# Performance work log

Hardware: AMD Instinct MI355X
Metric: run time of the kernel (lower is better)

The kernel has to match this reference:

```python
import jax, jax.numpy as jnp
import numpy as np

N = 100000        # nodes
E = 3200000       # edges (avg in-degree ~32)
NG = 64           # graphs in batch
F_IN = 64         # num_node_features
AVG_LOG = float(np.log(33.0))   # avg log-degree baked from deg (avg degree 32)
BN_EPS = 1e-5
STD_EPS = 1e-5

def _glorot(key, fi, fo):
    lim = float(np.sqrt(6.0 / (fi + fo)))
    return jax.random.uniform(key, (fi, fo), jnp.float32, -lim, lim)

def setup_inputs():
    key = jax.random.key(0)
    ks = jax.random.split(key, 16)
    inp = {
        'x': jax.random.normal(ks[0], (N, F_IN), jnp.float32),
        'edge_index': jax.random.randint(ks[1], (2, E), 0, N),
        'batch': jnp.sort(jax.random.randint(ks[2], (N,), 0, NG)),
    }
    dims = [(F_IN, 96), (96, 64), (64, 32), (32, 20)]
    for i, (fi, fo) in enumerate(dims):
        inp[f'w{i}'] = _glorot(ks[3 + i], 13 * fi, fo)  # (4 aggr * 3 scalers + 1 self) * F_in
        inp[f'b{i}'] = jnp.zeros((fo,), jnp.float32)
    for i, c in enumerate([96, 64, 20]):
        inp[f'g{i}'] = jnp.ones((c,), jnp.float32)
        inp[f'be{i}'] = jnp.zeros((c,), jnp.float32)
    inp['w_lin'] = _glorot(ks[10], 20, 11)
    inp['b_lin'] = jnp.zeros((11,), jnp.float32)
    return inp

def _pna_layer(x, src, dst, cnt, degc, W, b):
    m = x[src]                                          # [E, F] gather of neighbor feats
    inv = (1.0 / degc)[:, None]
    mean = jax.ops.segment_sum(m, dst, N) * inv
    mean_sq = jax.ops.segment_sum(m * m, dst, N) * inv
    std = jnp.sqrt(jax.nn.relu(mean_sq - mean * mean) + STD_EPS)
    has = (cnt > 0)[:, None]
    mn = jnp.where(has, jax.ops.segment_min(m, dst, N), 0.0)
    mx = jnp.where(has, jax.ops.segment_max(m, dst, N), 0.0)
    agg = jnp.concatenate([mean, mn, mx, std], axis=-1)  # [N, 4F]
    logd = jnp.log(degc + 1.0)[:, None]
    out = jnp.concatenate([agg, agg * (logd / AVG_LOG), agg * (AVG_LOG / logd)], axis=-1)  # [N, 12F]
    out = jnp.concatenate([x, out], axis=-1)             # [N, 13F] self + scaled aggregations
    return out @ W + b

def _bn(x, g, b):
    mu = x.mean(0)
    var = x.var(0)  # biased var: matches torch BatchNorm training forward
    return (x - mu) * jax.lax.rsqrt(var + BN_EPS) * g + b

def _forward(x, edge_index, batch, w0, b0, w1, b1, w2, b2, w3, b3,
             g0, be0, g1, be1, g2, be2, w_lin, b_lin):
    src, dst = edge_index[0], edge_index[1]
    cnt = jax.ops.segment_sum(jnp.ones((E,), x.dtype), dst, N)  # in-degree
    degc = jnp.maximum(cnt, 1.0)
    h = jax.nn.relu(_bn(_pna_layer(x, src, dst, cnt, degc, w0, b0), g0, be0))
    h = jax.nn.relu(_bn(_pna_layer(h, src, dst, cnt, degc, w1, b1), g1, be1))
    h = jax.nn.relu(_pna_layer(h, src, dst, cnt, degc, w2, b2))
    h = _bn(_pna_layer(h, src, dst, cnt, degc, w3, b3), g2, be2)
    gcnt = jnp.maximum(jax.ops.segment_sum(jnp.ones((N,), h.dtype), batch, NG), 1.0)
    z = jax.ops.segment_sum(h, batch, NG) / gcnt[:, None]       # global mean pool [NG, 20]
    out = jax.nn.softmax(z @ w_lin + b_lin, axis=-1)            # dropout identity (eval)
    return out, z

def reference(x, edge_index, batch, w0, b0, w1, b1, w2, b2, w3, b3,
              g0, be0, g1, be1, g2, be2, w_lin, b_lin):
    return _forward(x, edge_index, batch, w0, b0, w1, b1, w2, b2, w3, b3,
                    g0, be0, g1, be1, g2, be2, w_lin, b_lin)
```

## Files before the change

### kernel.cpp

```cpp
#include <hip/hip_runtime.h>

#define NN 100000
#define NGRAPH 64
#define NPART 8
#define NPB 12500
#define DB 16
#define PW_C 2048
#define AVGLOG 3.4965075614664802f

using f32x2 = __attribute__((ext_vector_type(2))) float;
using f32x4 = __attribute__((ext_vector_type(4))) float;
using f16x2 = __attribute__((ext_vector_type(2))) _Float16;
using f16x8 = __attribute__((ext_vector_type(8))) _Float16;
using f16x4 = __attribute__((ext_vector_type(4))) _Float16;
using i32x4 = __attribute__((ext_vector_type(4))) int;

__global__ __launch_bounds__(256) void k_pcnt(const int* __restrict__ ei,
                                              int* __restrict__ pcnt, int E, int W) {
  const int w = blockIdx.x * 4 + (threadIdx.x >> 6);
  const int lane = threadIdx.x & 63;
  if (w >= W) return;
  int c[NPART];
#pragma unroll
  for (int b = 0; b < NPART; ++b) c[b] = 0;
  const long long base = (long long)w * PW_C;
  for (int r = 0; r < PW_C / 256; ++r) {
    long long e0 = base + r * 256 + lane * 4;
    int bk[4] = {-1, -1, -1, -1};
    if (e0 + 3 < E) {
      i32x4 d = __builtin_nontemporal_load((const i32x4*)(ei + E + e0));
#pragma unroll
      for (int k = 0; k < 4; ++k) bk[k] = d[k] / NPB;
    } else {
#pragma unroll
      for (int k = 0; k < 4; ++k)
        if (e0 + k < E) bk[k] = ei[E + e0 + k] / NPB;
    }
#pragma unroll
    for (int b = 0; b < NPART; ++b) {
      int t = 0;
#pragma unroll
      for (int k = 0; k < 4; ++k) t += __popcll(__ballot(bk[k] == b));
      c[b] += t;
    }
  }
  if (lane == 0) {
#pragma unroll
    for (int b = 0; b < NPART; ++b) pcnt[w * NPART + b] = c[b];
  }
}

__global__ void k_pscan(const int* __restrict__ pcnt, int* __restrict__ pbase,
                        int* __restrict__ bcur, int W) {
  __shared__ int s[256];
  __shared__ int btot[NPART];
  const int t = threadIdx.x;
  const int per = (W + 255) / 256;
  for (int b = 0; b < NPART; ++b) {
    int loc = 0;
    const int w0 = t * per;
    for (int i = 0; i < per; ++i) {
      int w = w0 + i;
      if (w < W) loc += pcnt[w * NPART + b];
    }
    s[t] = loc;
    __syncthreads();
    for (int off = 1; off < 256; off <<= 1) {
      int u = (t >= off) ? s[t - off] : 0;
      __syncthreads();
      s[t] += u;
      __syncthreads();
    }
    int run = s[t] - loc;
    if (t == 255) btot[b] = s[255];
    for (int i = 0; i < per; ++i) {
      int w = w0 + i;
      if (w < W) {
        pbase[w * NPART + b] = run;
        run += pcnt[w * NPART + b];
      }
    }
    __syncthreads();
  }
  if (t < NPART) bcur[t] = btot[t];
}

__global__ __launch_bounds__(256) void k_pbin(const int* __restrict__ ei,
                                              const int* __restrict__ pbase,
                                              unsigned long long* __restrict__ bkt,
                                              int cap, int E, int W) {
  const int w = blockIdx.x * 4 + (threadIdx.x >> 6);
  const int lane = threadIdx.x & 63;
  if (w >= W) return;
  int off[NPART];
#pragma unroll
  for (int b = 0; b < NPART; ++b) off[b] = pbase[w * NPART + b];
  const unsigned long long lmask = (1ull << lane) - 1ull;
  const long long base = (long long)w * PW_C;
  for (int r = 0; r < PW_C / 256; ++r) {
    long long e0 = base + r * 256 + lane * 4;
    int bk[4] = {-1, -1, -1, -1};
    int sv[4], dv[4];
    if (e0 + 3 < E) {
      i32x4 d = __builtin_nontemporal_load((const i32x4*)(ei + E + e0));
      i32x4 s4 = __builtin_nontemporal_load((const i32x4*)(ei + e0));
#pragma unroll
      for (int k = 0; k < 4; ++k) { dv[k] = d[k]; sv[k] = s4[k]; bk[k] = d[k] / NPB; }
    } else {
#pragma unroll
      for (int k = 0; k < 4; ++k)
        if (e0 + k < E) { dv[k] = ei[E + e0 + k]; sv[k] = ei[e0 + k]; bk[k] = dv[k] / NPB; }
    }
#pragma unroll
    for (int k = 0; k < 4; ++k) {
#pragma unroll
      for (int b = 0; b < NPART; ++b) {
        unsigned long long m = __ballot(bk[k] == b);
        if (bk[k] == b) {
          int idx = off[b] + __popcll(m & lmask);
          bkt[(size_t)b * cap + idx] =
              ((unsigned long long)(unsigned)dv[k] << 32) | (unsigned)sv[k];
        }
        off[b] += __popcll(m);
      }
    }
  }
}

__global__ __launch_bounds__(256) void k_dhist(
    const unsigned long long* __restrict__ bkt, const int* __restrict__ bcur,
    int cap, int* __restrict__ dhist) {
  __shared__ int hist[NPB];
  const int p = blockIdx.x & (NPART - 1);
  const int b = blockIdx.x >> 3;
  const int tid = threadIdx.x;
  for (int i = tid; i < NPB; i += 256) hist[i] = 0;
  __syncthreads();
  const int n = bcur[p];
  const int chunk = (n + DB - 1) / DB;
  const int lo = b * chunk, hi = min(n, lo + chunk);
  const unsigned long long* base = bkt + (size_t)p * cap;
  const int plo = p * NPB;
  for (int i = lo + tid; i < hi; i += 256) {
    unsigned long long v = base[i];
    atomicAdd(&hist[(int)(v >> 32) - plo], 1);
  }
  __syncthreads();
  int* dst = dhist + ((size_t)p * DB + b) * NPB;
  for (int i = tid; i < NPB; i += 256) dst[i] = hist[i];
}

__global__ void k_mergesum(int* __restrict__ dhist, int* __restrict__ cnt,
                           int* __restrict__ bsum, int n) {
  __shared__ int s[256];
  int i = blockIdx.x * 256 + threadIdx.x;
  int acc = 0;
  if (i < n) {
    int p = i / NPB, li = i - p * NPB;
    int* hb = dhist + (size_t)p * DB * NPB + li;
#pragma unroll
    for (int b = 0; b < DB; ++b) {
      int t = hb[b * NPB];
      hb[b * NPB] = acc;
      acc += t;
    }
    cnt[i] = acc;
  }
  s[threadIdx.x] = acc;
  __syncthreads();
  for (int off = 128; off > 0; off >>= 1) {
    if (threadIdx.x < off) s[threadIdx.x] += s[threadIdx.x + off];
    __syncthreads();
  }
  if (threadIdx.x == 0) bsum[blockIdx.x] = s[0];
}

__global__ __launch_bounds__(256) void k_binfill(
    const unsigned long long* __restrict__ bkt, const int* __restrict__ bcur,
    int cap, const int* __restrict__ dhist, const int* __restrict__ row_ptr,
    int* __restrict__ colv) {
  __shared__ int rank[NPB];
  const int p = blockIdx.x & (NPART - 1);
  const int b = blockIdx.x >> 3;
  const int tid = threadIdx.x;
  const int plo = p * NPB;
  const int* soff = dhist + ((size_t)p * DB + b) * NPB;
  for (int li = tid; li < NPB; li += 256) rank[li] = row_ptr[plo + li] + soff[li];
  __syncthreads();
  const int n = bcur[p];
  const int chunk = (n + DB - 1) / DB;
  const int lo = b * chunk, hi = min(n, lo + chunk);
  const unsigned long long* base = bkt + (size_t)p * cap;
  for (int i = lo + tid; i < hi; i += 256) {
    unsigned long long v = base[i];
    int d = (int)(v >> 32);
    int s = (int)(v & 0xffffffffu);
    int pos = atomicAdd(&rank[d - plo], 1);
    colv[pos] = s;
  }
}

__global__ void k_scanb(const int* __restrict__ bsum, int* __restrict__ boff, int nb) {
  __shared__ int s[512];
  int t = threadIdx.x;
  int v = (t < nb) ? bsum[t] : 0;
  s[t] = v;
  __syncthreads();
  for (int off = 1; off < 512; off <<= 1) {
    int u = (t >= off) ? s[t - off] : 0;
    __syncthreads();
    s[t] += u;
    __syncthreads();
  }
  if (t < nb) boff[t] = s[t] - v;
}

__global__ void k_scatter(const int* __restrict__ cnt, const int* __restrict__ boff,
                          int* __restrict__ row_ptr, int n, int etot) {
  __shared__ int s[256];
  int i = blockIdx.x * 256 + threadIdx.x;
  int v = (i < n) ? cnt[i] : 0;
  s[threadIdx.x] = v;
  __syncthreads();
  for (int off = 1; off < 256; off <<= 1) {
    int u = (threadIdx.x >= off) ? s[threadIdx.x - off] : 0;
    __syncthreads();
    s[threadIdx.x] += u;
    __syncthreads();
  }
  if (i < n) row_ptr[i] = boff[blockIdx.x] + s[threadIdx.x] - v;
  if (i == 0) row_ptr[n] = etot;
}

__global__ void k_nodesc(const int* __restrict__ cnt, float* __restrict__ invd,
                         float* __restrict__ s1v, float* __restrict__ s2v, int n) {
  int i = blockIdx.x * 256 + threadIdx.x;
  if (i >= n) return;
  float degc = fmaxf((float)cnt[i], 1.f);
  invd[i] = 1.f / degc;
  float ld = logf(degc + 1.f);
  s1v[i] = ld * (1.f / AVGLOG);
  s2v[i] = AVGLOG / ld;
}

__global__ void k_wtprep(const float* __restrict__ W, _Float16* __restrict__ Wt,
                         int K, int FO, int FOP) {
  int i = blockIdx.x * 256 + threadIdx.x;
  if (i >= FOP * K) return;
  int nn = i / K, k = i - nn * K;
  float v = (nn < FO) ? W[k * FO + nn] : 0.f;
  int NT = FOP >> 4;
  int kt = k >> 5, q = (k >> 3) & 3, j = k & 7;
  int nt = nn >> 4, m = nn & 15;
  size_t idx = (((size_t)kt * NT + nt) * 64 + (q * 16 + m)) * 8 + j;
  Wt[idx] = (_Float16)v;
}

__global__ void k_xconv(const float* __restrict__ x, _Float16* __restrict__ x16, int n) {
  int i = blockIdx.x * 256 + threadIdx.x;
  if (i < n) x16[i] = (_Float16)x[i];
}

#define MFMA16(a, b, c) __builtin_amdgcn_mfma_f32_16x16x32_f16(a, b, c, 0, 0, 0)
#define TS 520

template <int F, int FO, int FOP, bool RELU, bool STATS, typename OT, int WPE>
__launch_bounds__(256, WPE)
__global__ void k_fused(const _Float16* __restrict__ hin,
                        const int* __restrict__ row_ptr, const int* __restrict__ colv,
                        const float* __restrict__ invd,
                        const float* __restrict__ s1g, const float* __restrict__ s2g,
                        const _Float16* __restrict__ Wt, const float* __restrict__ bias,
                        OT* __restrict__ hout, float* __restrict__ csum,
                        float* __restrict__ csq) {
  constexpr int F32 = F / 32;
  constexpr int KTA = F / 8;
  constexpr int NT = FOP / 16;
  constexpr int PPW = (2 * NT) / 4;
  constexpr int XW = F + 8;
  constexpr int SEG = F / 8;
  constexpr int NP = SEG / 2;
  __shared__ __align__(16) _Float16 s_x[32][XW];
  __shared__ __align__(16) _Float16 s_a[2 * KTA * TS];
  __shared__ float s_cs[2][FOP];

  const int tid = threadIdx.x;
  const int n0 = blockIdx.x * 32;

  for (int idx = tid; idx < 32 * (F / 8); idx += 256) {
    int rr = idx / (F / 8), cc = idx % (F / 8);
    *(f16x8*)&s_x[rr][8 * cc] = *(const f16x8*)&hin[(size_t)(n0 + rr) * F + 8 * cc];
  }
  if (STATS)
    for (int u = tid; u < 2 * FOP; u += 256) (&s_cs[0][0])[u] = 0.f;

  {
    const int r = tid >> 3, g = tid & 7;
    const int n = n0 + r;
    const int e0 = row_ptr[n], e1 = row_ptr[n + 1];
    f32x2 sm[NP], sq[NP];
    f16x2 mn[NP], mx[NP];
    const _Float16 HPI = __builtin_bit_cast(_Float16, (unsigned short)0x7C00);
    const _Float16 HNI = __builtin_bit_cast(_Float16, (unsigned short)0xFC00);
#pragma unroll
    for (int p = 0; p < NP; ++p) {
      sm[p] = (f32x2){0.f, 0.f};
      sq[p] = (f32x2){0.f, 0.f};
      mn[p] = (f16x2){HPI, HPI};
      mx[p] = (f16x2){HNI, HNI};
    }

    auto loadrow = [&](const _Float16* ra, f16x2* pr) {
      if constexpr (SEG % 8 == 0) {
#pragma unroll
        for (int c = 0; c < SEG / 8; ++c) {
          f16x8 v = ((const f16x8*)ra)[c];
          pr[4 * c + 0] = (f16x2){v[0], v[1]};
          pr[4 * c + 1] = (f16x2){v[2], v[3]};
          pr[4 * c + 2] = (f16x2){v[4], v[5]};
          pr[4 * c + 3] = (f16x2){v[6], v[7]};
        }
      } else {
#pragma unroll
        for (int c = 0; c < SEG / 4; ++c) {
          f16x4 v = ((const f16x4*)ra)[c];
          pr[2 * c + 0] = (f16x2){v[0], v[1]};
          pr[2 * c + 1] = (f16x2){v[2], v[3]};
        }
      }
    };
    auto accum = [&](const f16x2* pr) {
#pragma unroll
      for (int p = 0; p < NP; ++p) {
        f32x2 f = __builtin_convertvector(pr[p], f32x2);
        sm[p] += f;
        sq[p] += f * f;
        mn[p] = __builtin_elementwise_min(mn[p], pr[p]);
        mx[p] = __builtin_elementwise_max(mx[p], pr[p]);
      }
    };

    int e = e0;
    for (; e + 1 < e1; e += 2) {
      int c0 = __builtin_nontemporal_load(&colv[e]);
      int c1 = __builtin_nontemporal_load(&colv[e + 1]);
      f16x2 r0[NP], r1[NP];
      loadrow(hin + (size_t)c0 * F + g * SEG, r0);
      loadrow(hin + (size_t)c1 * F + g * SEG, r1);
      accum(r0);
      accum(r1);
    }
    if (e < e1) {
      int c0 = __builtin_nontemporal_load(&colv[e]);
      f16x2 r0[NP];
      loadrow(hin + (size_t)c0 * F + g * SEG, r0);
      accum(r0);
    }

    float iv = invd[n];
    bool has = (e1 > e0);
    const int m = r & 15;
    const int mt = r >> 4;
#pragma unroll
    for (int c = 0; c < SEG / 4; ++c) {
      f16x4 vals[4];
#pragma unroll
      for (int l = 0; l < 4; ++l) {
        int j = 4 * c + l;
        int p = j >> 1, k = j & 1;
        float mean = sm[p][k] * iv;
        float var = sq[p][k] * iv - mean * mean;
        float sd = sqrtf(fmaxf(var, 0.f) + 1e-5f);
        vals[0][l] = (_Float16)mean;
        vals[1][l] = has ? mn[p][k] : (_Float16)0.f;
        vals[2][l] = has ? mx[p][k] : (_Float16)0.f;
        vals[3][l] = (_Float16)sd;
      }
      int f0 = g * SEG + 4 * c;
#pragma unroll
      for (int a = 0; a < 4; ++a) {
        int kk0 = a * F + f0;
        int kt = kk0 >> 5, q = (kk0 >> 3) & 3, j0 = kk0 & 7;
        int ps = q * 16 + ((m + 2 * q) & 15);
        *(f16x4*)&s_a[((size_t)(mt * KTA + kt)) * TS + ps * 8 + j0] = vals[a];
      }
    }
  }
  __syncthreads();

  const int w = tid >> 6, ln = tid & 63;
  const int lm = ln & 15, q = ln >> 4;
  const int mt = w & 1;
  const int arow = mt * 16 + lm;
  const int aslot = (q * 16 + ((lm + 2 * q) & 15)) * 8;
  f32x4 acc0[PPW], acc1[PPW], acc2[PPW];
#pragma unroll
  for (int i = 0; i < PPW; ++i)
#pragma unroll
    for (int t = 0; t < 4; ++t) { acc0[i][t] = 0.f; acc1[i][t] = 0.f; acc2[i][t] = 0.f; }

#pragma unroll
  for (int kt = 0; kt < F32; ++kt) {
    f16x8 a = *(const f16x8*)&s_x[arow][kt * 32 + 8 * q];
#pragma unroll
    for (int i = 0; i < PPW; ++i) {
      int nt = (w >> 1) + 2 * i;
      f16x8 b = *(const f16x8*)&Wt[(((size_t)kt * NT + nt) * 64 + ln) * 8];
      acc0[i] = MFMA16(a, b, acc0[i]);
    }
  }
#pragma unroll
  for (int kt = 0; kt < KTA; ++kt) {
    f16x8 a = *(const f16x8*)&s_a[((size_t)(mt * KTA + kt)) * TS + aslot];
#pragma unroll
    for (int i = 0; i < PPW; ++i) {
      int nt = (w >> 1) + 2 * i;
      f16x8 b0 = *(const f16x8*)&Wt[(((size_t)(F32 + kt) * NT + nt) * 64 + ln) * 8];
      acc0[i] = MFMA16(a, b0, acc0[i]);
      f16x8 b1 = *(const f16x8*)&Wt[(((size_t)(F32 + KTA + kt) * NT + nt) * 64 + ln) * 8];
      acc1[i] = MFMA16(a, b1, acc1[i]);
      f16x8 b2 = *(const f16x8*)&Wt[(((size_t)(F32 + 2 * KTA + kt) * NT + nt) * 64 + ln) * 8];
      acc2[i] = MFMA16(a, b2, acc2[i]);
    }
  }

  float s1r[4], s2r[4];
#pragma unroll
  for (int t = 0; t < 4; ++t) {
    int node = n0 + mt * 16 + q * 4 + t;
    s1r[t] = s1g[node];
    s2r[t] = s2g[node];
  }
#pragma unroll
  for (int i = 0; i < PPW; ++i) {
    int nt = (w >> 1) + 2 * i;
    int ncol = nt * 16 + lm;
    if (FOP == FO || ncol < FO) {
      float bs = bias[ncol];
      float cs = 0.f, cq = 0.f;
#pragma unroll
      for (int t = 0; t < 4; ++t) {
        int node = n0 + mt * 16 + q * 4 + t;
        float v = acc0[i][t] + s1r[t] * acc1[i][t] + s2r[t] * acc2[i][t] + bs;
        if (RELU) v = fmaxf(v, 0.f);
        hout[(size_t)node * FO + ncol] = (OT)v;
        cs += v;
        cq += v * v;
      }
      if (STATS) {
        atomicAdd(&s_cs[0][ncol], cs);
        atomicAdd(&s_cs[1][ncol], cq);
      }
    }
  }
  if (STATS) {
    __syncthreads();
    if (tid < FO) {
      atomicAdd(&csum[tid], s_cs[0][tid]);
      atomicAdd(&csq[tid], s_cs[1][tid]);
    }
  }
}

__global__ void k_bn16(_Float16* __restrict__ h, const float* __restrict__ csum,
                       const float* __restrict__ csq, const float* __restrict__ gg,
                       const float* __restrict__ be, int n, int fo, int relu) {
  int i = blockIdx.x * 256 + threadIdx.x;
  int total = (n * fo) >> 3;
  if (i >= total) return;
  int c0 = (i << 3) % fo;
  float invn = 1.f / (float)n;
  f16x8 v = *(const f16x8*)&h[(size_t)i << 3];
  f16x8 o;
#pragma unroll
  for (int j = 0; j < 8; ++j) {
    int c = c0 + j;
    float mu = csum[c] * invn;
    float var = csq[c] * invn - mu * mu;
    float rs = rsqrtf(var + 1e-5f);
    float x = ((float)v[j] - mu) * rs * gg[c] + be[c];
    if (relu) x = fmaxf(x, 0.f);
    o[j] = (_Float16)x;
  }
  *(f16x8*)&h[(size_t)i << 3] = o;
}

__global__ void k_bnf(float* __restrict__ h, const float* __restrict__ csum,
                      const float* __restrict__ csq, const float* __restrict__ gg,
                      const float* __restrict__ be, int n, int fo, int relu) {
  int i = blockIdx.x * 256 + threadIdx.x;
  if (i >= n * fo) return;
  int c = i % fo;
  float invn = 1.f / (float)n;
  float mu = csum[c] * invn;
  float var = csq[c] * invn - mu * mu;
  float rs = rsqrtf(var + 1e-5f);
  float v = (h[i] - mu) * rs * gg[c] + be[c];
  if (relu) v = fmaxf(v, 0.f);
  h[i] = v;
}

__global__ void k_pool(const float* __restrict__ h, const int* __restrict__ batch,
                       float* __restrict__ zsum, float* __restrict__ gcnt, int n) {
  __shared__ float sv[NGRAPH * 20];
  __shared__ float sc[NGRAPH];
  int tid = threadIdx.x;
  for (int u = tid; u < NGRAPH * 20; u += 256) sv[u] = 0.f;
  if (tid < NGRAPH) sc[tid] = 0.f;
  __syncthreads();
  int i = blockIdx.x * 256 + tid;
  if (i < n) {
    int g = batch[i];
    atomicAdd(&sc[g], 1.f);
    for (int j = 0; j < 20; ++j) atomicAdd(&sv[g * 20 + j], h[(size_t)i * 20 + j]);
  }
  __syncthreads();
  if (tid < NGRAPH && sc[tid] != 0.f) {
    atomicAdd(&gcnt[tid], sc[tid]);
    for (int j = 0; j < 20; ++j) atomicAdd(&zsum[tid * 20 + j], sv[tid * 20 + j]);
  }
}

__global__ void k_head(const float* __restrict__ zsum, const float* __restrict__ gcnt,
                       const float* __restrict__ wl, const float* __restrict__ bl,
                       float* __restrict__ out) {
  int g = threadIdx.x;
  if (g >= NGRAPH) return;
  float z[20];
  float icg = 1.f / fmaxf(gcnt[g], 1.f);
#pragma unroll
  for (int j = 0; j < 20; ++j) {
    z[j] = zsum[g * 20 + j] * icg;
    out[NGRAPH * 11 + g * 20 + j] = z[j];
  }
  float lo[11];
#pragma unroll
  for (int o = 0; o < 11; ++o) {
    float a = bl[o];
    for (int j = 0; j < 20; ++j) a += z[j] * wl[j * 11 + o];
    lo[o] = a;
  }
  float m = lo[0];
  for (int o = 1; o < 11; ++o) m = fmaxf(m, lo[o]);
  float s = 0.f;
  for (int o = 0; o < 11; ++o) { lo[o] = expf(lo[o] - m); s += lo[o]; }
  float is = 1.f / s;
  for (int o = 0; o < 11; ++o) out[g * 11 + o] = lo[o] * is;
}

static inline char* carve(char*& p, size_t bytes) {
  char* r = p;
  p += (bytes + 255) & ~(size_t)255;
  return r;
}

extern "C" void kernel_launch(void* const* d_in, const int* in_sizes, int n_in,
                              void* d_out, int out_size, void* d_ws, size_t ws_size,
                              hipStream_t stream) {
  const float* x = (const float*)d_in[0];
  const int* ei = (const int*)d_in[1];
  const int* batch = (const int*)d_in[2];
  const float* W0 = (const float*)d_in[3];
  const float* b0 = (const float*)d_in[4];
  const float* W1 = (const float*)d_in[5];
  const float* b1 = (const float*)d_in[6];
  const float* W2 = (const float*)d_in[7];
  const float* b2 = (const float*)d_in[8];
  const float* W3 = (const float*)d_in[9];
  const float* b3 = (const float*)d_in[10];
  const float* g0 = (const float*)d_in[11];
  const float* be0 = (const float*)d_in[12];
  const float* g1 = (const float*)d_in[13];
  const float* be1 = (const float*)d_in[14];
  const float* g2 = (const float*)d_in[15];
  const float* be2 = (const float*)d_in[16];
  const float* wl = (const float*)d_in[17];
  const float* bl = (const float*)d_in[18];
  float* out = (float*)d_out;

  const int E = in_sizes[1] / 2;
  const int NB = (NN + 255) / 256;
  const int BCAP = E / NPART + 65536;
  const int W = (E + PW_C - 1) / PW_C;
  const int GB = (W + 3) / 4;

  char* p = (char*)d_ws;
  int* cnt = (int*)carve(p, (size_t)NN * 4);
  int* row_ptr = (int*)carve(p, (size_t)(NN + 1) * 4);
  int* bsum = (int*)carve(p, 2048);
  int* boff = (int*)carve(p, 2048);
  int* bcur = (int*)carve(p, 256);
  int* pcnt = (int*)carve(p, (size_t)W * NPART * 4);
  int* pbase = (int*)carve(p, (size_t)W * NPART * 4);
  int* colv = (int*)carve(p, (size_t)E * 4);
  unsigned long long* bkt = (unsigned long long*)carve(p, (size_t)NPART * BCAP * 8);
  int* dhist = (int*)carve(p, (size_t)NPART * DB * NPB * 4);
  float* invd = (float*)carve(p, (size_t)NN * 4);
  float* s1v = (float*)carve(p, (size_t)NN * 4);
  float* s2v = (float*)carve(p, (size_t)NN * 4);
  _Float16* Wt0 = (_Float16*)carve(p, (size_t)96 * 832 * 2);
  _Float16* Wt1 = (_Float16*)carve(p, (size_t)64 * 1248 * 2);
  _Float16* Wt2 = (_Float16*)carve(p, (size_t)32 * 832 * 2);
  _Float16* Wt3 = (_Float16*)carve(p, (size_t)32 * 416 * 2);
  float* cs = (float*)carve(p, 192 * 4);
  float* csum = cs;
  float* csq = cs + 96;
  float* pacc = (float*)carve(p, (NGRAPH * 20 + NGRAPH) * 4);
  float* zsum = pacc;
  float* gcnt = pacc + NGRAPH * 20;
  _Float16* x16 = (_Float16*)carve(p, (size_t)NN * 64 * 2);
  _Float16* hA16 = (_Float16*)carve(p, (size_t)NN * 96 * 2);
  _Float16* hB16 = (_Float16*)carve(p, (size_t)NN * 96 * 2);
  float* h3 = (float*)x16;

  hipMemsetAsync(pacc, 0, (NGRAPH * 20 + NGRAPH) * 4, stream);
  k_pcnt<<<GB, 256, 0, stream>>>(ei, pcnt, E, W);
  k_pscan<<<1, 256, 0, stream>>>(pcnt, pbase, bcur, W);
  k_pbin<<<GB, 256, 0, stream>>>(ei, pbase, bkt, BCAP, E, W);
  k_dhist<<<NPART * DB, 256, 0, stream>>>(bkt, bcur, BCAP, dhist);
  k_mergesum<<<NB, 256, 0, stream>>>(dhist, cnt, bsum, NN);
  k_scanb<<<1, 512, 0, stream>>>(bsum, boff, NB);
  k_scatter<<<NB, 256, 0, stream>>>(cnt, boff, row_ptr, NN, E);
  k_nodesc<<<NB, 256, 0, stream>>>(cnt, invd, s1v, s2v, NN);
  k_binfill<<<NPART * DB, 256, 0, stream>>>(bkt, bcur, BCAP, dhist, row_ptr, colv);

  k_wtprep<<<(96 * 832 + 255) / 256, 256, 0, stream>>>(W0, Wt0, 832, 96, 96);
  k_wtprep<<<(64 * 1248 + 255) / 256, 256, 0, stream>>>(W1, Wt1, 1248, 64, 64);
  k_wtprep<<<(32 * 832 + 255) / 256, 256, 0, stream>>>(W2, Wt2, 832, 32, 32);
  k_wtprep<<<(32 * 416 + 255) / 256, 256, 0, stream>>>(W3, Wt3, 416, 20, 32);
  k_xconv<<<(NN * 64 + 255) / 256, 256, 0, stream>>>(x, x16, NN * 64);

  const int GP = NN / 32;

  hipMemsetAsync(cs, 0, 192 * 4, stream);
  k_fused<64, 96, 96, false, true, _Float16, 6><<<GP, 256, 0, stream>>>(
      x16, row_ptr, colv, invd, s1v, s2v, Wt0, b0, hA16, csum, csq);
  k_bn16<<<(NN * 96 / 8 + 255) / 256, 256, 0, stream>>>(hA16, csum, csq, g0, be0, NN, 96, 1);

  hipMemsetAsync(cs, 0, 192 * 4, stream);
  k_fused<96, 64, 64, false, true, _Float16, 5><<<GP, 256, 0, stream>>>(
      hA16, row_ptr, colv, invd, s1v, s2v, Wt1, b1, hB16, csum, csq);
  k_bn16<<<(NN * 64 / 8 + 255) / 256, 256, 0, stream>>>(hB16, csum, csq, g1, be1, NN, 64, 1);

  k_fused<64, 32, 32, true, false, _Float16, 6><<<GP, 256, 0, stream>>>(
      hB16, row_ptr, colv, invd, s1v, s2v, Wt2, b2, hA16, csum, csq);

  hipMemsetAsync(cs, 0, 192 * 4, stream);
  k_fused<32, 20, 32, false, true, float, 8><<<GP, 256, 0, stream>>>(
      hA16, row_ptr, colv, invd, s1v, s2v, Wt3, b3, h3, csum, csq);
  k_bnf<<<(NN * 20 + 255) / 256, 256, 0, stream>>>(h3, csum, csq, g2, be2, NN, 20, 0);

  k_pool<<<NB, 256, 0, stream>>>(h3, batch, zsum, gcnt, NN);
  k_head<<<1, 64, 0, stream>>>(zsum, gcnt, wl, bl, out);
}
```

Measured before the change: 876.7 us.

## Halve aggregation LDS buffer by staging mean/min then max/std in two phases

The aggregated-feature tile in shared memory now holds only two of the four aggregations at a time. Mean and min are written, used for the first half of the MFMA K loop, then overwritten with max and std for the second half, with extra barriers between phases. The padded/swizzled layout (TS=520) is replaced by a plain 512 stride. Occupancy hints for layers 1 and 2 are raised to use the freed LDS, at the cost of keeping the accumulators live longer and possible LDS bank conflicts from dropping the swizzle.

```diff
diff --git a/kernel.cpp b/kernel.cpp
--- a/kernel.cpp
+++ b/kernel.cpp
@@ -262,7 +262,6 @@
 }
 
 #define MFMA16(a, b, c) __builtin_amdgcn_mfma_f32_16x16x32_f16(a, b, c, 0, 0, 0)
-#define TS 520
 
 template <int F, int FO, int FOP, bool RELU, bool STATS, typename OT, int WPE>
 __launch_bounds__(256, WPE)
@@ -275,13 +274,14 @@
                         float* __restrict__ csq) {
   constexpr int F32 = F / 32;
   constexpr int KTA = F / 8;
+  constexpr int KTH = KTA / 2;
   constexpr int NT = FOP / 16;
   constexpr int PPW = (2 * NT) / 4;
   constexpr int XW = F + 8;
   constexpr int SEG = F / 8;
   constexpr int NP = SEG / 2;
   __shared__ __align__(16) _Float16 s_x[32][XW];
-  __shared__ __align__(16) _Float16 s_a[2 * KTA * TS];
+  __shared__ __align__(16) _Float16 s_a[2 * KTH * 512];
   __shared__ float s_cs[2][FOP];
 
   const int tid = threadIdx.x;
@@ -294,12 +294,12 @@
   if (STATS)
     for (int u = tid; u < 2 * FOP; u += 256) (&s_cs[0][0])[u] = 0.f;
 
+  const int gr = tid >> 3, gg = tid & 7;
+  const int gn = n0 + gr;
+  const int ge0 = row_ptr[gn], ge1 = row_ptr[gn + 1];
+  f32x2 sm[NP], sq[NP];
+  f16x2 mn[NP], mx[NP];
   {
-    const int r = tid >> 3, g = tid & 7;
-    const int n = n0 + r;
-    const int e0 = row_ptr[n], e1 = row_ptr[n + 1];
-    f32x2 sm[NP], sq[NP];
-    f16x2 mn[NP], mx[NP];
     const _Float16 HPI = __builtin_bit_cast(_Float16, (unsigned short)0x7C00);
     const _Float16 HNI = __builtin_bit_cast(_Float16, (unsigned short)0xFC00);
 #pragma unroll
@@ -340,59 +340,67 @@
       }
     };
 
-    int e = e0;
-    for (; e + 1 < e1; e += 2) {
+    int e = ge0;
+    for (; e + 1 < ge1; e += 2) {
       int c0 = __builtin_nontemporal_load(&colv[e]);
       int c1 = __builtin_nontemporal_load(&colv[e + 1]);
       f16x2 r0[NP], r1[NP];
-      loadrow(hin + (size_t)c0 * F + g * SEG, r0);
-      loadrow(hin + (size_t)c1 * F + g * SEG, r1);
+      loadrow(hin + (size_t)c0 * F + gg * SEG, r0);
+      loadrow(hin + (size_t)c1 * F + gg * SEG, r1);
       accum(r0);
       accum(r1);
     }
-    if (e < e1) {
+    if (e < ge1) {
       int c0 = __builtin_nontemporal_load(&colv[e]);
       f16x2 r0[NP];
-      loadrow(hin + (size_t)c0 * F + g * SEG, r0);
+      loadrow(hin + (size_t)c0 * F + gg * SEG, r0);
       accum(r0);
     }
-
-    float iv = invd[n];
-    bool has = (e1 > e0);
-    const int m = r & 15;
-    const int mt = r >> 4;
+  }
+  const float giv = invd[gn];
+  const bool ghas = (ge1 > ge0);
+  const int gm = gr & 15;
+  const int gmt = gr >> 4;
+
+  auto write_half = [&](int phase) {
 #pragma unroll
     for (int c = 0; c < SEG / 4; ++c) {
-      f16x4 vals[4];
+      f16x4 v0, v1;
 #pragma unroll
       for (int l = 0; l < 4; ++l) {
         int j = 4 * c + l;
         int p = j >> 1, k = j & 1;
-        float mean = sm[p][k] * iv;
-        float var = sq[p][k] * iv - mean * mean;
-        float sd = sqrtf(fmaxf(var, 0.f) + 1e-5f);
-        vals[0][l] = (_Float16)mean;
-        vals[1][l] = has ? mn[p][k] : (_Float16)0.f;
-        vals[2][l] = has ? mx[p][k] : (_Float16)0.f;
-        vals[3][l] = (_Float16)sd;
-      }
-      int f0 = g * SEG + 4 * c;
-#pragma unroll
-      for (int a = 0; a < 4; ++a) {
+        if (phase == 0) {
+          float mean = sm[p][k] * giv;
+          v0[l] = (_Float16)mean;
+          v1[l] = ghas ? mn[p][k] : (_Float16)0.f;
+        } else {
+          float mean = sm[p][k] * giv;
+          float var = sq[p][k] * giv - mean * mean;
+          v0[l] = ghas ? mx[p][k] : (_Float16)0.f;
+          v1[l] = (_Float16)sqrtf(fmaxf(var, 0.f) + 1e-5f);
+        }
+      }
+      int f0 = gg * SEG + 4 * c;
+#pragma unroll
+      for (int aa = 0; aa < 2; ++aa) {
+        int a = phase * 2 + aa;
         int kk0 = a * F + f0;
-        int kt = kk0 >> 5, q = (kk0 >> 3) & 3, j0 = kk0 & 7;
-        int ps = q * 16 + ((m + 2 * q) & 15);
-        *(f16x4*)&s_a[((size_t)(mt * KTA + kt)) * TS + ps * 8 + j0] = vals[a];
-      }
-    }
-  }
+        int ktg = kk0 >> 5, q = (kk0 >> 3) & 3, j0 = kk0 & 7;
+        int ktl = ktg - phase * KTH;
+        *(f16x4*)&s_a[((size_t)(gmt * KTH + ktl)) * 512 + (q * 16 + gm) * 8 + j0] =
+            aa ? v1 : v0;
+      }
+    }
+  };
+
+  write_half(0);
   __syncthreads();
 
   const int w = tid >> 6, ln = tid & 63;
   const int lm = ln & 15, q = ln >> 4;
   const int mt = w & 1;
   const int arow = mt * 16 + lm;
-  const int aslot = (q * 16 + ((lm + 2 * q) & 15)) * 8;
   f32x4 acc0[PPW], acc1[PPW], acc2[PPW];
 #pragma unroll
   for (int i = 0; i < PPW; ++i)
@@ -410,8 +418,8 @@
     }
   }
 #pragma unroll
-  for (int kt = 0; kt < KTA; ++kt) {
-    f16x8 a = *(const f16x8*)&s_a[((size_t)(mt * KTA + kt)) * TS + aslot];
+  for (int kt = 0; kt < KTH; ++kt) {
+    f16x8 a = *(const f16x8*)&s_a[((size_t)(mt * KTH + kt)) * 512 + ln * 8];
 #pragma unroll
     for (int i = 0; i < PPW; ++i) {
       int nt = (w >> 1) + 2 * i;
@@ -420,6 +428,24 @@
       f16x8 b1 = *(const f16x8*)&Wt[(((size_t)(F32 + KTA + kt) * NT + nt) * 64 + ln) * 8];
       acc1[i] = MFMA16(a, b1, acc1[i]);
       f16x8 b2 = *(const f16x8*)&Wt[(((size_t)(F32 + 2 * KTA + kt) * NT + nt) * 64 + ln) * 8];
+      acc2[i] = MFMA16(a, b2, acc2[i]);
+    }
+  }
+  __syncthreads();
+  write_half(1);
+  __syncthreads();
+#pragma unroll
+  for (int kt = 0; kt < KTH; ++kt) {
+    int ktg = KTH + kt;
+    f16x8 a = *(const f16x8*)&s_a[((size_t)(mt * KTH + kt)) * 512 + ln * 8];
+#pragma unroll
+    for (int i = 0; i < PPW; ++i) {
+      int nt = (w >> 1) + 2 * i;
+      f16x8 b0 = *(const f16x8*)&Wt[(((size_t)(F32 + ktg) * NT + nt) * 64 + ln) * 8];
+      acc0[i] = MFMA16(a, b0, acc0[i]);
+      f16x8 b1 = *(const f16x8*)&Wt[(((size_t)(F32 + KTA + ktg) * NT + nt) * 64 + ln) * 8];
+      acc1[i] = MFMA16(a, b1, acc1[i]);
+      f16x8 b2 = *(const f16x8*)&Wt[(((size_t)(F32 + 2 * KTA + ktg) * NT + nt) * 64 + ln) * 8];
       acc2[i] = MFMA16(a, b2, acc2[i]);
     }
   }
@@ -638,11 +664,11 @@
   k_bn16<<<(NN * 96 / 8 + 255) / 256, 256, 0, stream>>>(hA16, csum, csq, g0, be0, NN, 96, 1);
 
   hipMemsetAsync(cs, 0, 192 * 4, stream);
-  k_fused<96, 64, 64, false, true, _Float16, 5><<<GP, 256, 0, stream>>>(
+  k_fused<96, 64, 64, false, true, _Float16, 6><<<GP, 256, 0, stream>>>(
       hA16, row_ptr, colv, invd, s1v, s2v, Wt1, b1, hB16, csum, csq);
   k_bn16<<<(NN * 64 / 8 + 255) / 256, 256, 0, stream>>>(hB16, csum, csq, g1, be1, NN, 64, 1);
 
-  k_fused<64, 32, 32, true, false, _Float16, 6><<<GP, 256, 0, stream>>>(
+  k_fused<64, 32, 32, true, false, _Float16, 8><<<GP, 256, 0, stream>>>(
       hB16, row_ptr, colv, invd, s1v, s2v, Wt2, b2, hA16, csum, csq);
 
   hipMemsetAsync(cs, 0, 192 * 4, stream);
```

After: 927.9 us. +5.8%, slower.
